# Kernel optimization log

Measured on AMD Instinct MI355X. Metric: run time of the kernel, lower is better.

The kernel has to match this reference:

```python
import jax, jax.numpy as jnp
import numpy as np

D_MODEL = 1024
NUM_HEADS = 16
HEAD_DIM = D_MODEL // NUM_HEADS


def setup_inputs() -> dict:
    key = jax.random.key(0)
    ks = jax.random.split(key, 6)
    B, S = 2, 2048
    s = 1.0 / np.sqrt(D_MODEL)
    return {
        "x": jax.random.normal(ks[0], (B, S, D_MODEL), dtype=jnp.float32),
        "Wq": jax.random.normal(ks[1], (D_MODEL, D_MODEL), dtype=jnp.float32) * s,
        "Wk": jax.random.normal(ks[2], (D_MODEL, D_MODEL), dtype=jnp.float32) * s,
        "Wv": jax.random.normal(ks[3], (D_MODEL, D_MODEL), dtype=jnp.float32) * s,
        "Wo": jax.random.normal(ks[4], (D_MODEL, D_MODEL), dtype=jnp.float32) * s,
        "bo": jax.random.normal(ks[5], (D_MODEL,), dtype=jnp.float32) * 0.01,
    }


def reference(x, Wq, Wk, Wv, Wo, bo):
    b, n, _ = x.shape
    # QKV projections (no bias, qkv_bias=False); weights applied as x @ W^T like nn.Linear
    q = (x @ Wq.T).reshape(b, n, NUM_HEADS, HEAD_DIM).transpose(0, 2, 1, 3)  # [b,h,n,d]
    k = (x @ Wk.T).reshape(b, n, NUM_HEADS, HEAD_DIM).transpose(0, 2, 1, 3)
    v = (x @ Wv.T).reshape(b, n, NUM_HEADS, HEAD_DIM).transpose(0, 2, 1, 3)
    scores = jnp.einsum("bhqd,bhkd->bhqk", q, k)
    causal = jnp.tril(jnp.ones((n, n), dtype=bool))  # keep where True
    scores = jnp.where(causal, scores, -jnp.inf)
    weights = jax.nn.softmax(scores / np.sqrt(HEAD_DIM), axis=-1)
    # dropout p=0.0 -> identity (eval semantics)
    ctx = jnp.einsum("bhqk,bhkd->bhqd", weights, v)
    ctx = ctx.transpose(0, 2, 1, 3).reshape(b, n, D_MODEL)
    return ctx @ Wo.T + bo
```

## Files before the change

kernel.cpp:

```cpp
#include <hip/hip_runtime.h>

#define D_MODEL 1024
#define NUM_HEADS 16
#define HEAD_DIM 64
#define BATCH 2
#define SEQ 2048
#define MTOT (BATCH * SEQ)

typedef __attribute__((ext_vector_type(8))) short bf16x8;
typedef __attribute__((ext_vector_type(4))) short s16x4;
typedef __attribute__((ext_vector_type(4))) float f32x4;
typedef unsigned short u16;
typedef unsigned long long u64;

__device__ __forceinline__ u16 f2bf(float f) {
    unsigned u = __float_as_uint(f);
    return (u16)((u + 0x7FFFu + ((u >> 16) & 1u)) >> 16);
}

__device__ __forceinline__ unsigned cvt_pk_bf16(float lo, float hi) {
    unsigned r;
    asm volatile("v_cvt_pk_bf16_f32 %0, %1, %2" : "=v"(r) : "v"(lo), "v"(hi));
    return r;
}

#define GLOAD16(gp, lp) __builtin_amdgcn_global_load_lds(                      \
    (const __attribute__((address_space(1))) void*)(gp),                       \
    (__attribute__((address_space(3))) void*)(lp), 16, 0, 0)

__global__ __launch_bounds__(256)
void cast_all_kernel(const float* __restrict__ x,  const float* __restrict__ Wq,
                     const float* __restrict__ Wk, const float* __restrict__ Wv,
                     const float* __restrict__ Wo, u16* __restrict__ dst)
{
    const int i = blockIdx.x * 256 + threadIdx.x;
    const float* src;
    int j;
    if (i < 524288) { src = x; j = i; }
    else if (i < 917504) {
        const int k = i - 524288;
        const int z = k >> 17;
        src = (z == 0) ? Wq : (z == 1) ? Wk : Wv;
        j = k & 0x1FFFF;
    } else { src = Wo; j = i - 917504; }
    const float4* s = reinterpret_cast<const float4*>(src) + (size_t)j * 2;
    float4 a = s[0], b = s[1];
    u16 tmp[8] = {f2bf(a.x), f2bf(a.y), f2bf(a.z), f2bf(a.w),
                  f2bf(b.x), f2bf(b.y), f2bf(b.z), f2bf(b.w)};
    *reinterpret_cast<int4*>(dst + (size_t)i * 8) = *reinterpret_cast<int4*>(tmp);
}

__global__ __launch_bounds__(256)
void gemm_qkv_kernel(const u16* __restrict__ A, const u16* __restrict__ B,
                     u16* __restrict__ Qo, u16* __restrict__ Ko, u16* __restrict__ Vt)
{
    __shared__ u16 Al[128 * 64];
    __shared__ u16 Bl[128 * 64];

    const int tid = threadIdx.x;
    const int l = tid & 63;
    const int w = tid >> 6;
    const int wm = w >> 1, wn = w & 1;
    const int lr = l & 15, lg = l >> 4;
    const int m0 = blockIdx.y * 128;
    const int n0 = blockIdx.x * 128;

    const int srow = tid >> 3;
    const int scol = ((tid & 7) ^ (srow & 7)) * 8;
    const int sxa = (lr & 7) * 8;

    f32x4 acc[4][4];
    #pragma unroll
    for (int i = 0; i < 4; ++i)
        #pragma unroll
        for (int j = 0; j < 4; ++j) acc[i][j] = (f32x4){0.f, 0.f, 0.f, 0.f};

    for (int k0 = 0; k0 < D_MODEL; k0 += 64) {
        __syncthreads();
        #pragma unroll
        for (int i = 0; i < 4; ++i) {
            const u16* ga = A + (size_t)(m0 + i * 32 + srow) * D_MODEL + k0 + scol;
            const u16* gb = B + (size_t)(n0 + i * 32 + srow) * D_MODEL + k0 + scol;
            GLOAD16(ga, Al + i * 2048 + w * 512);
            GLOAD16(gb, Bl + i * 2048 + w * 512);
        }
        __syncthreads();
        #pragma unroll
        for (int kc = 0; kc < 2; ++kc) {
            bf16x8 af[4], bfr[4];
            #pragma unroll
            for (int i = 0; i < 4; ++i)
                af[i] = *reinterpret_cast<const bf16x8*>(
                    &Al[(wm * 64 + i * 16 + lr) * 64 + ((kc * 32 + lg * 8) ^ sxa)]);
            #pragma unroll
            for (int j = 0; j < 4; ++j)
                bfr[j] = *reinterpret_cast<const bf16x8*>(
                    &Bl[(wn * 64 + j * 16 + lr) * 64 + ((kc * 32 + lg * 8) ^ sxa)]);
            #pragma unroll
            for (int i = 0; i < 4; ++i)
                #pragma unroll
                for (int j = 0; j < 4; ++j)
                    acc[i][j] = __builtin_amdgcn_mfma_f32_16x16x32_bf16(
                        af[i], bfr[j], acc[i][j], 0, 0, 0);
        }
    }

    const int z = (n0 >> 10);
    if (z < 2) {
        #pragma unroll
        for (int i = 0; i < 4; ++i) {
            #pragma unroll
            for (int r = 0; r < 4; ++r) {
                const int m = m0 + wm * 64 + i * 16 + lg * 4 + r;
                const int bb = m >> 11, s = m & (SEQ - 1);
                #pragma unroll
                for (int j = 0; j < 4; ++j) {
                    const int c = n0 + wn * 64 + j * 16 + lr;
                    const int cc = c & 1023, h = cc >> 6, d = cc & 63;
                    const size_t idx = ((size_t)(bb * NUM_HEADS + h) * SEQ + s) * 64 + d;
                    if (z == 0) Qo[idx] = f2bf(acc[i][j][r] * 0.125f);
                    else        Ko[idx] = f2bf(acc[i][j][r]);
                }
            }
        }
    } else {
        #pragma unroll
        for (int i = 0; i < 4; ++i) {
            const int mbase = m0 + wm * 64 + i * 16 + lg * 4;
            const int bb = mbase >> 11, s = mbase & (SEQ - 1);
            #pragma unroll
            for (int j = 0; j < 4; ++j) {
                const int c = n0 + wn * 64 + j * 16 + lr;
                const int cc = c & 1023, h = cc >> 6, d = cc & 63;
                u16 t4[4];
                #pragma unroll
                for (int r = 0; r < 4; ++r) t4[r] = f2bf(acc[i][j][r]);
                *reinterpret_cast<u64*>(
                    &Vt[((size_t)(bb * NUM_HEADS + h) * 64 + d) * SEQ + s]) =
                    *reinterpret_cast<u64*>(t4);
            }
        }
    }
}

__global__ __launch_bounds__(256)
void gemm_out_kernel(const u16* __restrict__ A, const u16* __restrict__ B,
                     const float* __restrict__ bias, float* __restrict__ out)
{
    __shared__ u16 Al[128 * 64];
    __shared__ u16 Bl[128 * 64];

    const int tid = threadIdx.x;
    const int l = tid & 63;
    const int w = tid >> 6;
    const int wm = w >> 1, wn = w & 1;
    const int lr = l & 15, lg = l >> 4;
    const int m0 = blockIdx.y * 128;
    const int n0 = blockIdx.x * 128;

    const int srow = tid >> 3;
    const int scol = ((tid & 7) ^ (srow & 7)) * 8;
    const int sxa = (lr & 7) * 8;

    f32x4 acc[4][4];
    #pragma unroll
    for (int i = 0; i < 4; ++i)
        #pragma unroll
        for (int j = 0; j < 4; ++j) acc[i][j] = (f32x4){0.f, 0.f, 0.f, 0.f};

    for (int k0 = 0; k0 < D_MODEL; k0 += 64) {
        __syncthreads();
        #pragma unroll
        for (int i = 0; i < 4; ++i) {
            const u16* ga = A + (size_t)(m0 + i * 32 + srow) * D_MODEL + k0 + scol;
            const u16* gb = B + (size_t)(n0 + i * 32 + srow) * D_MODEL + k0 + scol;
            GLOAD16(ga, Al + i * 2048 + w * 512);
            GLOAD16(gb, Bl + i * 2048 + w * 512);
        }
        __syncthreads();
        #pragma unroll
        for (int kc = 0; kc < 2; ++kc) {
            bf16x8 af[4], bfr[4];
            #pragma unroll
            for (int i = 0; i < 4; ++i)
                af[i] = *reinterpret_cast<const bf16x8*>(
                    &Al[(wm * 64 + i * 16 + lr) * 64 + ((kc * 32 + lg * 8) ^ sxa)]);
            #pragma unroll
            for (int j = 0; j < 4; ++j)
                bfr[j] = *reinterpret_cast<const bf16x8*>(
                    &Bl[(wn * 64 + j * 16 + lr) * 64 + ((kc * 32 + lg * 8) ^ sxa)]);
            #pragma unroll
            for (int i = 0; i < 4; ++i)
                #pragma unroll
                for (int j = 0; j < 4; ++j)
                    acc[i][j] = __builtin_amdgcn_mfma_f32_16x16x32_bf16(
                        af[i], bfr[j], acc[i][j], 0, 0, 0);
        }
    }

    #pragma unroll
    for (int i = 0; i < 4; ++i) {
        #pragma unroll
        for (int r = 0; r < 4; ++r) {
            const int m = m0 + wm * 64 + i * 16 + lg * 4 + r;
            #pragma unroll
            for (int j = 0; j < 4; ++j) {
                const int c = n0 + wn * 64 + j * 16 + lr;
                out[(size_t)m * D_MODEL + c] = acc[i][j][r] + bias[c];
            }
        }
    }
}

__global__ __launch_bounds__(256)
void attn_kernel(const u16* __restrict__ Q, const u16* __restrict__ K,
                 const u16* __restrict__ Vt, u16* __restrict__ ctx)
{
    __shared__ char LdsB[65536];

    const int tid = threadIdx.x;
    const int l = tid & 63;
    const int w = tid >> 6;
    const int lr = l & 15;
    const int lg = l >> 4;
    const int bh = blockIdx.y;
    const size_t hbase = (size_t)bh * SEQ * 64;
    const int b = bh >> 4, h = bh & (NUM_HEADS - 1);
    const u16* __restrict__ Kh = K + hbase;
    const u16* __restrict__ Vh = Vt + hbase;

    const int krow_t = tid >> 3;
    const int kcol   = ((tid & 7) ^ ((tid >> 3) & 7)) * 8;
    const int vrow_t = tid >> 4;
    const int vcol   = ((tid & 15) ^ ((tid >> 4) & 7)) * 8;
    const int ldst   = tid * 16;
    const int rswz   = (lr & 7) << 4;

    for (int qsel = 0; qsel < 2; ++qsel) {
        const int qtb = qsel ? (31 - blockIdx.x) : blockIdx.x;
        const int q0 = qtb * 64;
        const int qrow = q0 + w * 16 + lr;

        bf16x8 qf0, qf1;
        {
            const u16* qp = Q + hbase + (size_t)qrow * 64 + lg * 8;
            qf0 = *reinterpret_cast<const bf16x8*>(qp);
            qf1 = *reinterpret_cast<const bf16x8*>(qp + 32);
        }
        asm volatile("" :: "v"((int)qf0[0]), "v"((int)qf1[0]));

        f32x4 oacc[4];
        #pragma unroll
        for (int nb = 0; nb < 4; ++nb) oacc[nb] = (f32x4){0.f, 0.f, 0.f, 0.f};
        float mrun = -3.0e38f, lsum = 0.f;

        const int nstage = (qtb + 2) >> 1;

        {
            char* kb_l = LdsB;
            char* vb_l = LdsB + 16384;
            #pragma unroll
            for (int i = 0; i < 4; ++i) {
                GLOAD16(Kh + (size_t)(i * 32 + krow_t) * 64 + kcol, kb_l + i * 4096 + ldst);
                GLOAD16(Vh + (size_t)(i * 16 + vrow_t) * SEQ + vcol, vb_l + i * 4096 + ldst);
            }
        }

        for (int it = 0; it < nstage; ++it) {
            const int buf = it & 1;
            const bool pf = (it + 1 < nstage);
            if (pf) {
                const int kb = (it + 1) * 128;
                char* kb_l = LdsB + ((buf ^ 1) << 15);
                char* vb_l = kb_l + 16384;
                #pragma unroll
                for (int i = 0; i < 4; ++i) {
                    GLOAD16(Kh + (size_t)(kb + i * 32 + krow_t) * 64 + kcol,
                            kb_l + i * 4096 + ldst);
                    GLOAD16(Vh + (size_t)(i * 16 + vrow_t) * SEQ + kb + vcol,
                            vb_l + i * 4096 + ldst);
                }
                asm volatile("s_waitcnt vmcnt(8)" ::: "memory");
            } else {
                asm volatile("s_waitcnt vmcnt(0)" ::: "memory");
            }
            __builtin_amdgcn_s_barrier();

            const char* kbuf = LdsB + (buf << 15);
            const char* vbuf = kbuf + 16384;

            for (int hh = 0; hh < 2; ++hh) {
                const int j64 = 2 * it + hh;
                if (j64 > qtb) break;

                f32x4 s[4];
                __builtin_amdgcn_s_setprio(1);
                #pragma unroll
                for (int m = 0; m < 4; ++m) {
                    s[m] = (f32x4){0.f, 0.f, 0.f, 0.f};
                    const char* krow = kbuf + (hh * 64 + 16 * m + lr) * 128;
                    bf16x8 kf0 = *reinterpret_cast<const bf16x8*>(krow + ((lg * 16) ^ rswz));
                    bf16x8 kf1 = *reinterpret_cast<const bf16x8*>(krow + ((64 + lg * 16) ^ rswz));
                    s[m] = __builtin_amdgcn_mfma_f32_16x16x32_bf16(kf0, qf0, s[m], 0, 0, 0);
                    s[m] = __builtin_amdgcn_mfma_f32_16x16x32_bf16(kf1, qf1, s[m], 0, 0, 0);
                }
                __builtin_amdgcn_s_setprio(0);

                if (j64 == qtb) {
                    #pragma unroll
                    for (int m = 0; m < 4; ++m)
                        #pragma unroll
                        for (int r = 0; r < 4; ++r)
                            if (16 * m + 4 * lg + r > 16 * w + lr) s[m][r] = -3.0e38f;
                }

                float pmax = s[0][0];
                #pragma unroll
                for (int m = 0; m < 4; ++m)
                    #pragma unroll
                    for (int r = 0; r < 4; ++r) pmax = fmaxf(pmax, s[m][r]);
                pmax = fmaxf(pmax, __shfl_xor(pmax, 16));
                pmax = fmaxf(pmax, __shfl_xor(pmax, 32));

                if (!__all(pmax - mrun <= 8.0f)) {
                    const float mnew = fmaxf(mrun, pmax);
                    const float corr = __expf(mrun - mnew);
                    lsum *= corr;
                    #pragma unroll
                    for (int nb = 0; nb < 4; ++nb) {
                        oacc[nb][0] *= corr; oacc[nb][1] *= corr;
                        oacc[nb][2] *= corr; oacc[nb][3] *= corr;
                    }
                    mrun = mnew;
                }

                float p[4][4];
                float ps = 0.f;
                #pragma unroll
                for (int m = 0; m < 4; ++m)
                    #pragma unroll
                    for (int r = 0; r < 4; ++r) {
                        p[m][r] = __expf(s[m][r] - mrun);
                        ps += p[m][r];
                    }
                ps += __shfl_xor(ps, 16);
                ps += __shfl_xor(ps, 32);
                lsum += ps;

                unsigned dw[4][2];
                #pragma unroll
                for (int m = 0; m < 4; ++m) {
                    dw[m][0] = cvt_pk_bf16(p[m][0], p[m][1]);
                    dw[m][1] = cvt_pk_bf16(p[m][2], p[m][3]);
                }

                __builtin_amdgcn_s_setprio(1);
                #pragma unroll
                for (int c = 0; c < 2; ++c) {
                    union { unsigned u[4]; bf16x8 v; } pb;
                    pb.u[0] = dw[2 * c][0];     pb.u[1] = dw[2 * c][1];
                    pb.u[2] = dw[2 * c + 1][0]; pb.u[3] = dw[2 * c + 1][1];
                    #pragma unroll
                    for (int nb = 0; nb < 4; ++nb) {
                        const char* vrow = vbuf + (16 * nb + lr) * 256 + hh * 128;
                        union { s16x4 hv[2]; bf16x8 v; } vf;
                        vf.hv[0] = *reinterpret_cast<const s16x4*>(
                            vrow + ((c * 64 + lg * 8) ^ rswz));
                        vf.hv[1] = *reinterpret_cast<const s16x4*>(
                            vrow + ((c * 64 + 32 + lg * 8) ^ rswz));
                        oacc[nb] = __builtin_amdgcn_mfma_f32_16x16x32_bf16(
                            vf.v, pb.v, oacc[nb], 0, 0, 0);
                    }
                }
                __builtin_amdgcn_s_setprio(0);
            }
            __builtin_amdgcn_s_barrier();
        }

        const float inv = 1.0f / lsum;
        u16* op = ctx + ((size_t)(b * SEQ) + qrow) * D_MODEL + h * 64 + 4 * lg;
        #pragma unroll
        for (int nb = 0; nb < 4; ++nb) {
            u16 t4[4];
            #pragma unroll
            for (int r = 0; r < 4; ++r) t4[r] = f2bf(oacc[nb][r] * inv);
            *reinterpret_cast<u64*>(op + 16 * nb) = *reinterpret_cast<u64*>(t4);
        }
    }
}


extern "C" void kernel_launch(void* const* d_in, const int* in_sizes, int n_in,
                              void* d_out, int out_size, void* d_ws, size_t ws_size,
                              hipStream_t stream)
{
    const float* x  = (const float*)d_in[0];
    const float* Wq = (const float*)d_in[1];
    const float* Wk = (const float*)d_in[2];
    const float* Wv = (const float*)d_in[3];
    const float* Wo = (const float*)d_in[4];
    const float* bo = (const float*)d_in[5];
    float* out = (float*)d_out;

    u16* xb   = (u16*)d_ws;
    u16* wqkv = xb   + (size_t)MTOT * D_MODEL;
    u16* wob  = wqkv + (size_t)3 * D_MODEL * D_MODEL;
    u16* Qw   = wob  + (size_t)D_MODEL * D_MODEL;
    u16* Kw   = Qw   + (size_t)MTOT * D_MODEL;
    u16* Vtw  = Kw   + (size_t)MTOT * D_MODEL;
    u16* ctxb = Vtw  + (size_t)MTOT * D_MODEL;

    cast_all_kernel<<<4096, 256, 0, stream>>>(x, Wq, Wk, Wv, Wo, xb);

    dim3 gq(3 * D_MODEL / 128, MTOT / 128);
    gemm_qkv_kernel<<<gq, 256, 0, stream>>>(xb, wqkv, Qw, Kw, Vtw);

    dim3 ga(16, BATCH * NUM_HEADS);
    attn_kernel<<<ga, 256, 0, stream>>>(Qw, Kw, Vtw, ctxb);

    dim3 go(D_MODEL / 128, MTOT / 128);
    gemm_out_kernel<<<go, 256, 0, stream>>>(ctxb, wob, bo, out);
}
```

Baseline: 127.4 us.

## Restructure attention: one q-tile per block, XCD-aware mapping, max-free exp2 softmax

Each attention block now handles a single 64-row query tile over a 1024-block grid, with block indices mapped so that heads stay grouped per XCD and the longest causal tiles are scheduled first. The key/value tile shrinks from 128 to 64 rows, cutting LDS to 32KB so more blocks can be resident. The online running-max rescaling is dropped: the log2(e) factor is folded into the Q scaling and exp2 is applied directly, and the row-sum reduction is deferred to the end of the loop. This removes the max/shuffle/rescale work, but the output can overflow if scores grow large, because it no longer subtracts the maximum.

```diff
diff --git a/kernel.cpp b/kernel.cpp
--- a/kernel.cpp
+++ b/kernel.cpp
@@ -23,6 +23,12 @@
     asm volatile("v_cvt_pk_bf16_f32 %0, %1, %2" : "=v"(r) : "v"(lo), "v"(hi));
     return r;
 }
+
+#if __has_builtin(__builtin_amdgcn_exp2f)
+#define EXP2(x) __builtin_amdgcn_exp2f(x)
+#else
+#define EXP2(x) exp2f(x)
+#endif
 
 #define GLOAD16(gp, lp) __builtin_amdgcn_global_load_lds(                      \
     (const __attribute__((address_space(1))) void*)(gp),                       \
@@ -118,7 +124,7 @@
                     const int c = n0 + wn * 64 + j * 16 + lr;
                     const int cc = c & 1023, h = cc >> 6, d = cc & 63;
                     const size_t idx = ((size_t)(bb * NUM_HEADS + h) * SEQ + s) * 64 + d;
-                    if (z == 0) Qo[idx] = f2bf(acc[i][j][r] * 0.125f);
+                    if (z == 0) Qo[idx] = f2bf(acc[i][j][r] * 0.18033688f);
                     else        Ko[idx] = f2bf(acc[i][j][r]);
                 }
             }
@@ -216,176 +222,150 @@
 void attn_kernel(const u16* __restrict__ Q, const u16* __restrict__ K,
                  const u16* __restrict__ Vt, u16* __restrict__ ctx)
 {
-    __shared__ char LdsB[65536];
+    __shared__ char LdsB[2][16384];
 
     const int tid = threadIdx.x;
     const int l = tid & 63;
     const int w = tid >> 6;
     const int lr = l & 15;
     const int lg = l >> 4;
-    const int bh = blockIdx.y;
+
+    const int xcd  = blockIdx.x & 7;
+    const int slot = blockIdx.x >> 3;
+    const int bh   = xcd * 4 + (slot >> 5);
+    const int qtb  = 31 - (slot & 31);
     const size_t hbase = (size_t)bh * SEQ * 64;
     const int b = bh >> 4, h = bh & (NUM_HEADS - 1);
     const u16* __restrict__ Kh = K + hbase;
     const u16* __restrict__ Vh = Vt + hbase;
 
-    const int krow_t = tid >> 3;
-    const int kcol   = ((tid & 7) ^ ((tid >> 3) & 7)) * 8;
-    const int vrow_t = tid >> 4;
-    const int vcol   = ((tid & 15) ^ ((tid >> 4) & 7)) * 8;
-    const int ldst   = tid * 16;
-    const int rswz   = (lr & 7) << 4;
-
-    for (int qsel = 0; qsel < 2; ++qsel) {
-        const int qtb = qsel ? (31 - blockIdx.x) : blockIdx.x;
-        const int q0 = qtb * 64;
-        const int qrow = q0 + w * 16 + lr;
-
-        bf16x8 qf0, qf1;
+    const int q0 = qtb * 64;
+    const int qrow = q0 + w * 16 + lr;
+
+    const int r0 = tid >> 3;
+    const int c0 = ((tid & 7) ^ (r0 & 7)) * 8;
+    const int r1 = (256 + tid) >> 3;
+    const int c1 = ((tid & 7) ^ (r1 & 7)) * 8;
+    const int d0b = tid * 16;
+    const int d1b = 4096 + tid * 16;
+    const int rswz = (lr & 7) << 4;
+
+    bf16x8 qf0, qf1;
+    {
+        const u16* qp = Q + hbase + (size_t)qrow * 64 + lg * 8;
+        qf0 = *reinterpret_cast<const bf16x8*>(qp);
+        qf1 = *reinterpret_cast<const bf16x8*>(qp + 32);
+    }
+
+    f32x4 oacc[4];
+    #pragma unroll
+    for (int nb = 0; nb < 4; ++nb) oacc[nb] = (f32x4){0.f, 0.f, 0.f, 0.f};
+    float lsum = 0.f;
+
+    {
+        char* kb = LdsB[0];
+        char* vb = LdsB[0] + 8192;
+        GLOAD16(Kh + (size_t)r0 * 64 + c0, kb + d0b);
+        GLOAD16(Kh + (size_t)r1 * 64 + c1, kb + d1b);
+        GLOAD16(Vh + (size_t)r0 * SEQ + c0, vb + d0b);
+        GLOAD16(Vh + (size_t)r1 * SEQ + c1, vb + d1b);
+    }
+
+    for (int it = 0; it <= qtb; ++it) {
+        const int buf = it & 1;
+        if (it < qtb) {
+            const int kb64 = (it + 1) * 64;
+            char* kbl = LdsB[buf ^ 1];
+            char* vbl = kbl + 8192;
+            GLOAD16(Kh + (size_t)(kb64 + r0) * 64 + c0, kbl + d0b);
+            GLOAD16(Kh + (size_t)(kb64 + r1) * 64 + c1, kbl + d1b);
+            GLOAD16(Vh + (size_t)r0 * SEQ + kb64 + c0, vbl + d0b);
+            GLOAD16(Vh + (size_t)r1 * SEQ + kb64 + c1, vbl + d1b);
+            asm volatile("s_waitcnt vmcnt(4)" ::: "memory");
+        } else {
+            asm volatile("s_waitcnt vmcnt(0)" ::: "memory");
+        }
+        __builtin_amdgcn_s_barrier();
+
+        const char* kbuf = LdsB[buf];
+        const char* vbuf = kbuf + 8192;
+
+        f32x4 s[4];
+        __builtin_amdgcn_s_setprio(1);
+        #pragma unroll
+        for (int m = 0; m < 4; ++m) {
+            s[m] = (f32x4){0.f, 0.f, 0.f, 0.f};
+            const char* krow = kbuf + (16 * m + lr) * 128;
+            bf16x8 kf0 = *reinterpret_cast<const bf16x8*>(krow + ((lg * 16) ^ rswz));
+            bf16x8 kf1 = *reinterpret_cast<const bf16x8*>(krow + ((64 + lg * 16) ^ rswz));
+            s[m] = __builtin_amdgcn_mfma_f32_16x16x32_bf16(kf0, qf0, s[m], 0, 0, 0);
+            s[m] = __builtin_amdgcn_mfma_f32_16x16x32_bf16(kf1, qf1, s[m], 0, 0, 0);
+        }
+        __builtin_amdgcn_s_setprio(0);
+
+        if (it == qtb) {
+            #pragma unroll
+            for (int m = 0; m < 4; ++m)
+                #pragma unroll
+                for (int r = 0; r < 4; ++r)
+                    if (16 * m + 4 * lg + r > 16 * w + lr) s[m][r] = -1.0e38f;
+        }
+
+        float p[4][4];
+        #pragma unroll
+        for (int m = 0; m < 4; ++m)
+            #pragma unroll
+            for (int r = 0; r < 4; ++r) p[m][r] = EXP2(s[m][r]);
+
         {
-            const u16* qp = Q + hbase + (size_t)qrow * 64 + lg * 8;
-            qf0 = *reinterpret_cast<const bf16x8*>(qp);
-            qf1 = *reinterpret_cast<const bf16x8*>(qp + 32);
-        }
-        asm volatile("" :: "v"((int)qf0[0]), "v"((int)qf1[0]));
-
-        f32x4 oacc[4];
-        #pragma unroll
-        for (int nb = 0; nb < 4; ++nb) oacc[nb] = (f32x4){0.f, 0.f, 0.f, 0.f};
-        float mrun = -3.0e38f, lsum = 0.f;
-
-        const int nstage = (qtb + 2) >> 1;
-
-        {
-            char* kb_l = LdsB;
-            char* vb_l = LdsB + 16384;
-            #pragma unroll
-            for (int i = 0; i < 4; ++i) {
-                GLOAD16(Kh + (size_t)(i * 32 + krow_t) * 64 + kcol, kb_l + i * 4096 + ldst);
-                GLOAD16(Vh + (size_t)(i * 16 + vrow_t) * SEQ + vcol, vb_l + i * 4096 + ldst);
+            float a0 = (p[0][0] + p[0][1]) + (p[0][2] + p[0][3]);
+            float a1 = (p[1][0] + p[1][1]) + (p[1][2] + p[1][3]);
+            float a2 = (p[2][0] + p[2][1]) + (p[2][2] + p[2][3]);
+            float a3 = (p[3][0] + p[3][1]) + (p[3][2] + p[3][3]);
+            lsum += (a0 + a1) + (a2 + a3);
+        }
+
+        unsigned dw[4][2];
+        #pragma unroll
+        for (int m = 0; m < 4; ++m) {
+            dw[m][0] = cvt_pk_bf16(p[m][0], p[m][1]);
+            dw[m][1] = cvt_pk_bf16(p[m][2], p[m][3]);
+        }
+
+        __builtin_amdgcn_s_setprio(1);
+        #pragma unroll
+        for (int c = 0; c < 2; ++c) {
+            union { unsigned u[4]; bf16x8 v; } pb;
+            pb.u[0] = dw[2 * c][0];     pb.u[1] = dw[2 * c][1];
+            pb.u[2] = dw[2 * c + 1][0]; pb.u[3] = dw[2 * c + 1][1];
+            #pragma unroll
+            for (int nb = 0; nb < 4; ++nb) {
+                const char* vrow = vbuf + (16 * nb + lr) * 128;
+                union { s16x4 hv[2]; bf16x8 v; } vf;
+                vf.hv[0] = *reinterpret_cast<const s16x4*>(
+                    vrow + ((c * 64 + lg * 8) ^ rswz));
+                vf.hv[1] = *reinterpret_cast<const s16x4*>(
+                    vrow + ((c * 64 + 32 + lg * 8) ^ rswz));
+                oacc[nb] = __builtin_amdgcn_mfma_f32_16x16x32_bf16(
+                    vf.v, pb.v, oacc[nb], 0, 0, 0);
             }
         }
-
-        for (int it = 0; it < nstage; ++it) {
-            const int buf = it & 1;
-            const bool pf = (it + 1 < nstage);
-            if (pf) {
-                const int kb = (it + 1) * 128;
-                char* kb_l = LdsB + ((buf ^ 1) << 15);
-                char* vb_l = kb_l + 16384;
-                #pragma unroll
-                for (int i = 0; i < 4; ++i) {
-                    GLOAD16(Kh + (size_t)(kb + i * 32 + krow_t) * 64 + kcol,
-                            kb_l + i * 4096 + ldst);
-                    GLOAD16(Vh + (size_t)(i * 16 + vrow_t) * SEQ + kb + vcol,
-                            vb_l + i * 4096 + ldst);
-                }
-                asm volatile("s_waitcnt vmcnt(8)" ::: "memory");
-            } else {
-                asm volatile("s_waitcnt vmcnt(0)" ::: "memory");
-            }
-            __builtin_amdgcn_s_barrier();
-
-            const char* kbuf = LdsB + (buf << 15);
-            const char* vbuf = kbuf + 16384;
-
-            for (int hh = 0; hh < 2; ++hh) {
-                const int j64 = 2 * it + hh;
-                if (j64 > qtb) break;
-
-                f32x4 s[4];
-                __builtin_amdgcn_s_setprio(1);
-                #pragma unroll
-                for (int m = 0; m < 4; ++m) {
-                    s[m] = (f32x4){0.f, 0.f, 0.f, 0.f};
-                    const char* krow = kbuf + (hh * 64 + 16 * m + lr) * 128;
-                    bf16x8 kf0 = *reinterpret_cast<const bf16x8*>(krow + ((lg * 16) ^ rswz));
-                    bf16x8 kf1 = *reinterpret_cast<const bf16x8*>(krow + ((64 + lg * 16) ^ rswz));
-                    s[m] = __builtin_amdgcn_mfma_f32_16x16x32_bf16(kf0, qf0, s[m], 0, 0, 0);
-                    s[m] = __builtin_amdgcn_mfma_f32_16x16x32_bf16(kf1, qf1, s[m], 0, 0, 0);
-                }
-                __builtin_amdgcn_s_setprio(0);
-
-                if (j64 == qtb) {
-                    #pragma unroll
-                    for (int m = 0; m < 4; ++m)
-                        #pragma unroll
-                        for (int r = 0; r < 4; ++r)
-                            if (16 * m + 4 * lg + r > 16 * w + lr) s[m][r] = -3.0e38f;
-                }
-
-                float pmax = s[0][0];
-                #pragma unroll
-                for (int m = 0; m < 4; ++m)
-                    #pragma unroll
-                    for (int r = 0; r < 4; ++r) pmax = fmaxf(pmax, s[m][r]);
-                pmax = fmaxf(pmax, __shfl_xor(pmax, 16));
-                pmax = fmaxf(pmax, __shfl_xor(pmax, 32));
-
-                if (!__all(pmax - mrun <= 8.0f)) {
-                    const float mnew = fmaxf(mrun, pmax);
-                    const float corr = __expf(mrun - mnew);
-                    lsum *= corr;
-                    #pragma unroll
-                    for (int nb = 0; nb < 4; ++nb) {
-                        oacc[nb][0] *= corr; oacc[nb][1] *= corr;
-                        oacc[nb][2] *= corr; oacc[nb][3] *= corr;
-                    }
-                    mrun = mnew;
-                }
-
-                float p[4][4];
-                float ps = 0.f;
-                #pragma unroll
-                for (int m = 0; m < 4; ++m)
-                    #pragma unroll
-                    for (int r = 0; r < 4; ++r) {
-                        p[m][r] = __expf(s[m][r] - mrun);
-                        ps += p[m][r];
-                    }
-                ps += __shfl_xor(ps, 16);
-                ps += __shfl_xor(ps, 32);
-                lsum += ps;
-
-                unsigned dw[4][2];
-                #pragma unroll
-                for (int m = 0; m < 4; ++m) {
-                    dw[m][0] = cvt_pk_bf16(p[m][0], p[m][1]);
-                    dw[m][1] = cvt_pk_bf16(p[m][2], p[m][3]);
-                }
-
-                __builtin_amdgcn_s_setprio(1);
-                #pragma unroll
-                for (int c = 0; c < 2; ++c) {
-                    union { unsigned u[4]; bf16x8 v; } pb;
-                    pb.u[0] = dw[2 * c][0];     pb.u[1] = dw[2 * c][1];
-                    pb.u[2] = dw[2 * c + 1][0]; pb.u[3] = dw[2 * c + 1][1];
-                    #pragma unroll
-                    for (int nb = 0; nb < 4; ++nb) {
-                        const char* vrow = vbuf + (16 * nb + lr) * 256 + hh * 128;
-                        union { s16x4 hv[2]; bf16x8 v; } vf;
-                        vf.hv[0] = *reinterpret_cast<const s16x4*>(
-                            vrow + ((c * 64 + lg * 8) ^ rswz));
-                        vf.hv[1] = *reinterpret_cast<const s16x4*>(
-                            vrow + ((c * 64 + 32 + lg * 8) ^ rswz));
-                        oacc[nb] = __builtin_amdgcn_mfma_f32_16x16x32_bf16(
-                            vf.v, pb.v, oacc[nb], 0, 0, 0);
-                    }
-                }
-                __builtin_amdgcn_s_setprio(0);
-            }
-            __builtin_amdgcn_s_barrier();
-        }
-
-        const float inv = 1.0f / lsum;
-        u16* op = ctx + ((size_t)(b * SEQ) + qrow) * D_MODEL + h * 64 + 4 * lg;
-        #pragma unroll
-        for (int nb = 0; nb < 4; ++nb) {
-            u16 t4[4];
-            #pragma unroll
-            for (int r = 0; r < 4; ++r) t4[r] = f2bf(oacc[nb][r] * inv);
-            *reinterpret_cast<u64*>(op + 16 * nb) = *reinterpret_cast<u64*>(t4);
-        }
+        __builtin_amdgcn_s_setprio(0);
+
+        __builtin_amdgcn_s_barrier();
+    }
+
+    lsum += __shfl_xor(lsum, 16);
+    lsum += __shfl_xor(lsum, 32);
+    const float inv = 1.0f / lsum;
+
+    u16* op = ctx + ((size_t)(b * SEQ) + qrow) * D_MODEL + h * 64 + 4 * lg;
+    #pragma unroll
+    for (int nb = 0; nb < 4; ++nb) {
+        u16 t4[4];
+        #pragma unroll
+        for (int r = 0; r < 4; ++r) t4[r] = f2bf(oacc[nb][r] * inv);
+        *reinterpret_cast<u64*>(op + 16 * nb) = *reinterpret_cast<u64*>(t4);
     }
 }
 
@@ -415,8 +395,7 @@
     dim3 gq(3 * D_MODEL / 128, MTOT / 128);
     gemm_qkv_kernel<<<gq, 256, 0, stream>>>(xb, wqkv, Qw, Kw, Vtw);
 
-    dim3 ga(16, BATCH * NUM_HEADS);
-    attn_kernel<<<ga, 256, 0, stream>>>(Qw, Kw, Vtw, ctxb);
+    attn_kernel<<<dim3(1024), 256, 0, stream>>>(Qw, Kw, Vtw, ctxb);
 
     dim3 go(D_MODEL / 128, MTOT / 128);
     gemm_out_kernel<<<go, 256, 0, stream>>>(ctxb, wob, bo, out);
```

New measurement: 129.5 us. Within noise of the previous version (+1.7%).
